# Kernel tuning notes

Hardware: AMD Instinct MI355X
Metric: run time of the kernel (lower is better)

## Reference

```python
import jax, jax.numpy as jnp
import numpy as np

N, E, F_IN, F_HID, F_EMB, N_CLS = 50000, 800000, 100, 100, 64, 40


def setup_inputs() -> dict:
    key = jax.random.key(0)
    ks = jax.random.split(key, 8)
    x = jax.random.normal(ks[0], (N, F_IN), dtype=jnp.float32)
    edge_index = jax.random.randint(ks[1], (2, E), 0, N, dtype=jnp.int32)
    W1 = jax.random.normal(ks[2], (F_IN, F_HID), dtype=jnp.float32) / np.sqrt(F_IN)
    b1 = jnp.zeros((F_HID,), dtype=jnp.float32)
    W2 = jax.random.normal(ks[3], (F_HID, F_EMB), dtype=jnp.float32) / np.sqrt(F_HID)
    b2 = jnp.zeros((F_EMB,), dtype=jnp.float32)
    Wc = jax.random.normal(ks[4], (F_EMB, N_CLS), dtype=jnp.float32) / np.sqrt(F_EMB)
    bc = jnp.zeros((N_CLS,), dtype=jnp.float32)
    return {"x": x, "edge_index": edge_index, "W1": W1, "b1": b1,
            "W2": W2, "b2": b2, "Wc": Wc, "bc": bc}


def _gcn_conv(x, W, b, src, dst, dinv):
    # linear transform then symmetric-normalized neighbor aggregation
    h = x @ W                                   # [N, out]
    norm = dinv[src] * dinv[dst]                # [E+N]
    msg = h[src] * norm[:, None]                # gather + scale (edge-wise)
    out = jax.ops.segment_sum(msg, dst, num_segments=x.shape[0])
    return out + b


def reference(x, edge_index, W1, b1, W2, b2, Wc, bc):
    x = x.astype(jnp.float32)
    n = x.shape[0]
    loop = jnp.arange(n, dtype=edge_index.dtype)
    src = jnp.concatenate([edge_index[0], loop])  # add self-loops (PyG GCNConv)
    dst = jnp.concatenate([edge_index[1], loop])
    # degree (with self-loops) and D^-1/2, shared by both conv layers
    deg = jax.ops.segment_sum(jnp.ones_like(dst, dtype=x.dtype), dst, num_segments=n)
    dinv = jnp.where(deg > 0, jax.lax.rsqrt(jnp.maximum(deg, 1e-12)), 0.0)
    h = jax.nn.relu(_gcn_conv(x, W1, b1, src, dst, dinv))   # dropout off (eval)
    h = _gcn_conv(h, W2, b2, src, dst, dinv)
    h = jax.nn.relu(h)                                      # dropout off (eval)
    return h @ Wc + bc
```

## Files before the change

### kernel.cpp

```cpp
#include <hip/hip_runtime.h>

#define FIN 100
#define FHID 100
#define FEMB 64
#define NCLS 40

#define BSH 6
#define NSEG 8
#define SEGCAP 224
#define CSTR 16

typedef __attribute__((ext_vector_type(8))) short short8;
typedef __attribute__((ext_vector_type(4))) float f32x4;

__device__ inline unsigned short f2bf(float f) {
    unsigned u = __float_as_uint(f);
    u += 0x7FFFu + ((u >> 16) & 1u);
    return (unsigned short)(u >> 16);
}
__device__ inline float bf2f(unsigned short s) {
    return __uint_as_float((unsigned)s << 16);
}
__device__ inline float4 bf4(ushort4 u) {
    return make_float4(bf2f(u.x), bf2f(u.y), bf2f(u.z), bf2f(u.w));
}

__global__ __launch_bounds__(256) void k_bucket_sort(const int* __restrict__ arena,
                                                     const int* __restrict__ cur,
                                                     int* __restrict__ gcounter,
                                                     int* __restrict__ rowptr,
                                                     int* __restrict__ rowend,
                                                     float* __restrict__ dinv,
                                                     int* __restrict__ src_sorted, int n) {
    const int b = blockIdx.x;
    __shared__ int cnt[64], off[64];
    __shared__ int base_sh;
    if (threadIdx.x < 64) cnt[threadIdx.x] = 0;
    __syncthreads();
    for (int s = 0; s < NSEG; ++s) {
        int len = cur[(b * NSEG + s) * CSTR];
        if (len > SEGCAP) len = SEGCAP;
        const int* seg = arena + (size_t)(b * NSEG + s) * SEGCAP;
        for (int idx = threadIdx.x; idx < len; idx += 256)
            atomicAdd(&cnt[seg[idx] & 63], 1);
    }
    __syncthreads();
    if (threadIdx.x == 0) {
        int run = 0;
        for (int j = 0; j < 64; ++j) { off[j] = run; run += cnt[j]; }
        base_sh = atomicAdd(gcounter, run);
    }
    __syncthreads();
    const int base = base_sh;
    if (threadIdx.x < 64) {
        int node = (b << BSH) + threadIdx.x;
        if (node < n) {
            int r0 = base + off[threadIdx.x];
            rowptr[node] = r0;
            rowend[node] = r0 + cnt[threadIdx.x];
            dinv[node] = rsqrtf((float)cnt[threadIdx.x] + 1.0f);
        }
    }
    __syncthreads();
    for (int s = 0; s < NSEG; ++s) {
        int len = cur[(b * NSEG + s) * CSTR];
        if (len > SEGCAP) len = SEGCAP;
        const int* seg = arena + (size_t)(b * NSEG + s) * SEGCAP;
        for (int idx = threadIdx.x; idx < len; idx += 256) {
            int v = seg[idx];
            int lpos = atomicAdd(&off[v & 63], 1);
            src_sorted[base + lpos] = v >> BSH;
        }
    }
}

template <int KIN, int KOUT, int NTY, bool A_BF16, bool BIAS, bool OUT_BF16, bool SCATTER>
__global__ __launch_bounds__(256) void k_gemm_mfma(const void* __restrict__ A,
                                                   const float* __restrict__ W,
                                                   const float* __restrict__ bias,
                                                   void* __restrict__ C, int n,
                                                   const int* __restrict__ src,
                                                   const int* __restrict__ dst,
                                                   int* __restrict__ cur,
                                                   int* __restrict__ arena, int E) {
    constexpr int KP    = ((KIN + 31) / 32) * 32;
    constexpr int NTALL = (KOUT + 15) / 16;
    constexpr int NTC   = NTY * 16;
    constexpr int APAD  = KP + 8;
    constexpr int NKC   = KP / 32;
    constexpr int TQ    = (NTY + 1) / 2;
    constexpr int KQ4   = KIN / 4;

    __shared__ unsigned short Abf[128 * APAD];
    __shared__ unsigned short Wt[NTC * APAD];

    const int row0 = blockIdx.x * 128;
    const int tid = threadIdx.x;

    if constexpr (SCATTER) {
        const int stride = gridDim.x * 256;
        for (int e = blockIdx.x * 256 + tid; e < E; e += stride) {
            int d = dst[e];
            int b = d >> BSH;
            int slot = b * NSEG + ((e >> 8) & (NSEG - 1));
            int p = atomicAdd(&cur[slot * CSTR], 1);
            if (p < SEGCAP) arena[slot * SEGCAP + p] = (src[e] << BSH) | (d & 63);
        }
    }

    if constexpr (A_BF16) {
        const ushort4* A4 = (const ushort4*)A;
        for (int idx = tid; idx < 128 * KQ4; idx += 256) {
            int r = idx / KQ4;
            int kq = idx - r * KQ4;
            ushort4 v = make_ushort4(0, 0, 0, 0);
            if (row0 + r < n) v = A4[(size_t)(row0 + r) * KQ4 + kq];
            *(ushort4*)&Abf[r * APAD + kq * 4] = v;
        }
    } else {
        const float* Af = (const float*)A;
        for (int idx = tid; idx < 128 * KQ4; idx += 256) {
            int r = idx / KQ4;
            int kq = idx - r * KQ4;
            float4 v = make_float4(0.f, 0.f, 0.f, 0.f);
            if (row0 + r < n) v = ((const float4*)(Af + (size_t)(row0 + r) * KIN))[kq];
            ushort4 o;
            o.x = f2bf(v.x); o.y = f2bf(v.y); o.z = f2bf(v.z); o.w = f2bf(v.w);
            *(ushort4*)&Abf[r * APAD + kq * 4] = o;
        }
    }
    if (KP > KIN) {
        constexpr int PADW = (KP > KIN) ? (KP - KIN) : 1;
        for (int idx = tid; idx < 128 * PADW; idx += 256) {
            int r = idx / PADW;
            Abf[r * APAD + KIN + (idx - r * PADW)] = 0;
        }
    }

    const int lane = tid & 63;
    const int w    = tid >> 6;
    const int m0   = (w >> 1) * 64;
    const int t0   = (w & 1) * TQ;
    const int lm   = lane & 15;
    const int quad = lane >> 4;

    for (int tb = 0; tb < NTALL; tb += NTY) {
        const int ntloc = (NTALL - tb < NTY) ? (NTALL - tb) : NTY;

        for (int idx = tid; idx < KIN * NTC; idx += 256) {
            int k = idx / NTC;
            int c = idx - k * NTC;
            int gc = tb * 16 + c;
            float v = (gc < KOUT) ? W[(size_t)k * KOUT + gc] : 0.f;
            Wt[c * APAD + k] = f2bf(v);
        }
        if (KP > KIN) {
            constexpr int PADW = (KP > KIN) ? (KP - KIN) : 1;
            for (int idx = tid; idx < NTC * PADW; idx += 256) {
                int c = idx / PADW;
                Wt[c * APAD + KIN + (idx - c * PADW)] = 0;
            }
        }
        __syncthreads();

        const int tcnt = (ntloc - t0 < TQ) ? (ntloc - t0) : TQ;

        f32x4 acc[4][TQ];
        #pragma unroll
        for (int i = 0; i < 4; ++i)
            #pragma unroll
            for (int t = 0; t < TQ; ++t)
                acc[i][t] = (f32x4)(0.f);

        for (int kt = 0; kt < NKC; ++kt) {
            short8 a[4], b[TQ];
            #pragma unroll
            for (int i = 0; i < 4; ++i)
                a[i] = *(const short8*)&Abf[(m0 + i * 16 + lm) * APAD + kt * 32 + quad * 8];
            #pragma unroll
            for (int t = 0; t < TQ; ++t)
                if (t < tcnt)
                    b[t] = *(const short8*)&Wt[((t0 + t) * 16 + lm) * APAD + kt * 32 + quad * 8];
            #pragma unroll
            for (int i = 0; i < 4; ++i)
                #pragma unroll
                for (int t = 0; t < TQ; ++t)
                    if (t < tcnt)
                        acc[i][t] = __builtin_amdgcn_mfma_f32_16x16x32_bf16(a[i], b[t], acc[i][t], 0, 0, 0);
        }

        #pragma unroll
        for (int t = 0; t < TQ; ++t) {
            if (t >= tcnt) continue;
            int col = (tb + t0 + t) * 16 + lm;
            if (col >= KOUT) continue;
            float bv = BIAS ? bias[col] : 0.f;
            #pragma unroll
            for (int i = 0; i < 4; ++i) {
                #pragma unroll
                for (int rg = 0; rg < 4; ++rg) {
                    int row = row0 + m0 + i * 16 + quad * 4 + rg;
                    if (row < n) {
                        float v = acc[i][t][rg] + bv;
                        if (OUT_BF16)
                            ((unsigned short*)C)[(size_t)row * KOUT + col] = f2bf(v);
                        else
                            ((float*)C)[(size_t)row * KOUT + col] = v;
                    }
                }
            }
        }
        __syncthreads();
    }
}

template <int F>
__global__ __launch_bounds__(256) void k_agg_bf(const unsigned short* __restrict__ h,
                                                const int* __restrict__ rowptr,
                                                const int* __restrict__ rowend,
                                                const int* __restrict__ src_sorted,
                                                const float* __restrict__ dinv,
                                                const float* __restrict__ bias,
                                                unsigned short* __restrict__ out, int n) {
    const int G = F / 4;
    int gid = blockIdx.x * blockDim.x + threadIdx.x;
    if (gid >= n * G) return;
    int i = gid / G;
    int cq = gid % G;
    const ushort4* h4 = (const ushort4*)h;

    float4 acc = make_float4(0.f, 0.f, 0.f, 0.f);
    int e = rowptr[i];
    const int end = rowend[i];
    for (; e + 3 < end; e += 4) {
        int s0 = src_sorted[e];
        int s1 = src_sorted[e + 1];
        int s2 = src_sorted[e + 2];
        int s3 = src_sorted[e + 3];
        ushort4 u0 = h4[(size_t)s0 * G + cq];
        ushort4 u1 = h4[(size_t)s1 * G + cq];
        ushort4 u2 = h4[(size_t)s2 * G + cq];
        ushort4 u3 = h4[(size_t)s3 * G + cq];
        float n0 = dinv[s0], n1 = dinv[s1], n2 = dinv[s2], n3 = dinv[s3];
        float4 v0 = bf4(u0), v1 = bf4(u1), v2 = bf4(u2), v3 = bf4(u3);
        acc.x = fmaf(v0.x, n0, acc.x); acc.y = fmaf(v0.y, n0, acc.y);
        acc.z = fmaf(v0.z, n0, acc.z); acc.w = fmaf(v0.w, n0, acc.w);
        acc.x = fmaf(v1.x, n1, acc.x); acc.y = fmaf(v1.y, n1, acc.y);
        acc.z = fmaf(v1.z, n1, acc.z); acc.w = fmaf(v1.w, n1, acc.w);
        acc.x = fmaf(v2.x, n2, acc.x); acc.y = fmaf(v2.y, n2, acc.y);
        acc.z = fmaf(v2.z, n2, acc.z); acc.w = fmaf(v2.w, n2, acc.w);
        acc.x = fmaf(v3.x, n3, acc.x); acc.y = fmaf(v3.y, n3, acc.y);
        acc.z = fmaf(v3.z, n3, acc.z); acc.w = fmaf(v3.w, n3, acc.w);
    }
    for (; e < end; ++e) {
        int s0 = src_sorted[e];
        float n0 = dinv[s0];
        float4 v0 = bf4(h4[(size_t)s0 * G + cq]);
        acc.x = fmaf(v0.x, n0, acc.x); acc.y = fmaf(v0.y, n0, acc.y);
        acc.z = fmaf(v0.z, n0, acc.z); acc.w = fmaf(v0.w, n0, acc.w);
    }

    float d = dinv[i];
    float4 hv = bf4(h4[(size_t)i * G + cq]);
    float4 bv = *(const float4*)&bias[cq * 4];
    ushort4 st;
    st.x = f2bf(fmaxf(fmaf(d, fmaf(d, hv.x, acc.x), bv.x), 0.f));
    st.y = f2bf(fmaxf(fmaf(d, fmaf(d, hv.y, acc.y), bv.y), 0.f));
    st.z = f2bf(fmaxf(fmaf(d, fmaf(d, hv.z, acc.z), bv.z), 0.f));
    st.w = f2bf(fmaxf(fmaf(d, fmaf(d, hv.w, acc.w), bv.w), 0.f));
    ((ushort4*)out)[(size_t)i * G + cq] = st;
}

extern "C" void kernel_launch(void* const* d_in, const int* in_sizes, int n_in,
                              void* d_out, int out_size, void* d_ws, size_t ws_size,
                              hipStream_t stream) {
    const float* x  = (const float*)d_in[0];
    const int*   ei = (const int*)d_in[1];
    const float* W1 = (const float*)d_in[2];
    const float* b1 = (const float*)d_in[3];
    const float* W2 = (const float*)d_in[4];
    const float* b2 = (const float*)d_in[5];
    const float* Wc = (const float*)d_in[6];
    const float* bc = (const float*)d_in[7];
    float* out = (float*)d_out;

    const int N = in_sizes[0] / FIN;
    const int E = in_sizes[1] / 2;
    const int* src = ei;
    const int* dst = ei + E;
    const int NBK = (N + 63) >> BSH;

    auto align = [](size_t v) { return (v + 255) & ~(size_t)255; };
    char* ws = (char*)d_ws;
    const size_t cur_bytes = align((size_t)NBK * NSEG * CSTR * 4 + 256);
    int*   cur        = (int*)ws;   ws += cur_bytes;
    int*   gcounter   = cur + (size_t)NBK * NSEG * CSTR;
    int*   arena      = (int*)ws;   ws += align((size_t)NBK * NSEG * SEGCAP * 4);
    int*   rowptr     = (int*)ws;   ws += align((size_t)N * 4);
    int*   rowend     = (int*)ws;   ws += align((size_t)N * 4);
    int*   src_sorted = (int*)ws;   ws += align((size_t)E * 4);
    float* dinv       = (float*)ws; ws += align((size_t)N * 4);
    unsigned short* h1  = (unsigned short*)ws; ws += align((size_t)N * FHID * 2);
    unsigned short* a1r = (unsigned short*)ws; ws += align((size_t)N * FHID * 2);
    unsigned short* h2  = (unsigned short*)ws; ws += align((size_t)N * FEMB * 2);
    unsigned short* a2r = (unsigned short*)ws; ws += align((size_t)N * FEMB * 2);

    const int B = 256;
    const int nmb = (N + 127) / 128;

    hipMemsetAsync(cur, 0, cur_bytes, stream);

    k_gemm_mfma<FIN, FHID, 4, false, false, true, true><<<nmb, B, 0, stream>>>(
        x, W1, nullptr, h1, N, src, dst, cur, arena, E);

    k_bucket_sort<<<NBK, B, 0, stream>>>(arena, cur, gcounter, rowptr, rowend, dinv, src_sorted, N);

    k_agg_bf<FHID><<<((size_t)N * (FHID / 4) + B - 1) / B, B, 0, stream>>>(
        h1, rowptr, rowend, src_sorted, dinv, b1, a1r, N);

    k_gemm_mfma<FHID, FEMB, 4, true, false, true, false><<<nmb, B, 0, stream>>>(
        a1r, W2, nullptr, h2, N, nullptr, nullptr, nullptr, nullptr, 0);

    k_agg_bf<FEMB><<<((size_t)N * (FEMB / 4) + B - 1) / B, B, 0, stream>>>(
        h2, rowptr, rowend, src_sorted, dinv, b2, a2r, N);

    k_gemm_mfma<FEMB, NCLS, 4, true, true, false, false><<<nmb, B, 0, stream>>>(
        a2r, Wc, bc, out, N, nullptr, nullptr, nullptr, nullptr, 0);
}
```

Before: 225.4 us.

## Replace fused per-edge global-atomic scatter with LDS-binned super-bucket scatter kernel

Edge binning moves out of the first GEMM into a dedicated kernel. Each block bins 2048 edges into 256-node super-buckets using shared-memory counters, then reserves space in the global arena with one atomic per bucket and writes records back coalesced. The bucket sort now processes one 256-node super-bucket per block, using a parallel prefix scan instead of a serial loop. The aim is to cut global atomic contention and scattered writes, at the cost of an extra launch and the loss of overlap between scattering and the GEMM. Capacity limits of 4608 per super-bucket could drop edges if degrees are skewed.

```diff
diff --git a/kernel.cpp b/kernel.cpp
--- a/kernel.cpp
+++ b/kernel.cpp
@@ -5,10 +5,11 @@
 #define FEMB 64
 #define NCLS 40
 
-#define BSH 6
-#define NSEG 8
-#define SEGCAP 224
+#define SBSH 8
+#define CAPB 24
+#define SBCAP 4608
 #define CSTR 16
+#define EPB 2048
 
 typedef __attribute__((ext_vector_type(8))) short short8;
 typedef __attribute__((ext_vector_type(4))) float f32x4;
@@ -25,64 +26,110 @@
     return make_float4(bf2f(u.x), bf2f(u.y), bf2f(u.z), bf2f(u.w));
 }
 
+__global__ __launch_bounds__(256) void k_scatter_bin(const int* __restrict__ src,
+                                                     const int* __restrict__ dst,
+                                                     int* __restrict__ gcur,
+                                                     int* __restrict__ arena,
+                                                     int E, int nsb) {
+    __shared__ int bins[256 * CAPB];
+    __shared__ int bcnt[256];
+    __shared__ int pbase[256];
+    const int tid = threadIdx.x;
+    bcnt[tid] = 0;
+    __syncthreads();
+
+    const int e0 = blockIdx.x * EPB;
+    #pragma unroll
+    for (int k = 0; k < EPB / 256; ++k) {
+        int e = e0 + k * 256 + tid;
+        if (e < E) {
+            int d = dst[e];
+            int sb = d >> SBSH;
+            int rec = (src[e] << SBSH) | (d & 255);
+            int c = atomicAdd(&bcnt[sb], 1);
+            if (c < CAPB) {
+                bins[sb * CAPB + c] = rec;
+            } else {
+                int p = atomicAdd(&gcur[sb * CSTR], 1);
+                if (p < SBCAP) arena[(size_t)sb * SBCAP + p] = rec;
+            }
+        }
+    }
+    __syncthreads();
+
+    if (tid < nsb) {
+        int c = bcnt[tid];
+        if (c > CAPB) c = CAPB;
+        pbase[tid] = (c > 0) ? atomicAdd(&gcur[tid * CSTR], c) : 0;
+    }
+    __syncthreads();
+
+    const int wv = tid >> 6, lane = tid & 63;
+    for (int sb = wv; sb < nsb; sb += 4) {
+        int c = bcnt[sb];
+        if (c > CAPB) c = CAPB;
+        int p = pbase[sb];
+        if (lane < c && p + lane < SBCAP)
+            arena[(size_t)sb * SBCAP + p + lane] = bins[sb * CAPB + lane];
+    }
+}
+
 __global__ __launch_bounds__(256) void k_bucket_sort(const int* __restrict__ arena,
-                                                     const int* __restrict__ cur,
+                                                     const int* __restrict__ gcur,
                                                      int* __restrict__ gcounter,
                                                      int* __restrict__ rowptr,
                                                      int* __restrict__ rowend,
                                                      float* __restrict__ dinv,
                                                      int* __restrict__ src_sorted, int n) {
-    const int b = blockIdx.x;
-    __shared__ int cnt[64], off[64];
+    const int sb = blockIdx.x;
+    const int tid = threadIdx.x;
+    __shared__ int cnt[256], off[256], tmp[256];
     __shared__ int base_sh;
-    if (threadIdx.x < 64) cnt[threadIdx.x] = 0;
-    __syncthreads();
-    for (int s = 0; s < NSEG; ++s) {
-        int len = cur[(b * NSEG + s) * CSTR];
-        if (len > SEGCAP) len = SEGCAP;
-        const int* seg = arena + (size_t)(b * NSEG + s) * SEGCAP;
-        for (int idx = threadIdx.x; idx < len; idx += 256)
-            atomicAdd(&cnt[seg[idx] & 63], 1);
-    }
-    __syncthreads();
-    if (threadIdx.x == 0) {
-        int run = 0;
-        for (int j = 0; j < 64; ++j) { off[j] = run; run += cnt[j]; }
-        base_sh = atomicAdd(gcounter, run);
-    }
-    __syncthreads();
+    cnt[tid] = 0;
+    __syncthreads();
+
+    int len = gcur[sb * CSTR];
+    if (len > SBCAP) len = SBCAP;
+    const int* seg = arena + (size_t)sb * SBCAP;
+    for (int i = tid; i < len; i += 256)
+        atomicAdd(&cnt[seg[i] & 255], 1);
+    __syncthreads();
+
+    const int v = cnt[tid];
+    tmp[tid] = v;
+    __syncthreads();
+    for (int o = 1; o < 256; o <<= 1) {
+        int t = (tid >= o) ? tmp[tid - o] : 0;
+        __syncthreads();
+        tmp[tid] += t;
+        __syncthreads();
+    }
+    off[tid] = tmp[tid] - v;
+    if (tid == 255) base_sh = atomicAdd(gcounter, tmp[255]);
+    __syncthreads();
+
     const int base = base_sh;
-    if (threadIdx.x < 64) {
-        int node = (b << BSH) + threadIdx.x;
-        if (node < n) {
-            int r0 = base + off[threadIdx.x];
-            rowptr[node] = r0;
-            rowend[node] = r0 + cnt[threadIdx.x];
-            dinv[node] = rsqrtf((float)cnt[threadIdx.x] + 1.0f);
-        }
-    }
-    __syncthreads();
-    for (int s = 0; s < NSEG; ++s) {
-        int len = cur[(b * NSEG + s) * CSTR];
-        if (len > SEGCAP) len = SEGCAP;
-        const int* seg = arena + (size_t)(b * NSEG + s) * SEGCAP;
-        for (int idx = threadIdx.x; idx < len; idx += 256) {
-            int v = seg[idx];
-            int lpos = atomicAdd(&off[v & 63], 1);
-            src_sorted[base + lpos] = v >> BSH;
-        }
-    }
-}
-
-template <int KIN, int KOUT, int NTY, bool A_BF16, bool BIAS, bool OUT_BF16, bool SCATTER>
+    int node = (sb << SBSH) + tid;
+    if (node < n) {
+        int r0 = base + off[tid];
+        rowptr[node] = r0;
+        rowend[node] = r0 + v;
+        dinv[node] = rsqrtf((float)v + 1.0f);
+    }
+    __syncthreads();
+
+    for (int i = tid; i < len; i += 256) {
+        int rec = seg[i];
+        int lpos = atomicAdd(&off[rec & 255], 1);
+        src_sorted[base + lpos] = rec >> SBSH;
+    }
+}
+
+template <int KIN, int KOUT, int NTY, bool A_BF16, bool BIAS, bool OUT_BF16>
 __global__ __launch_bounds__(256) void k_gemm_mfma(const void* __restrict__ A,
                                                    const float* __restrict__ W,
                                                    const float* __restrict__ bias,
-                                                   void* __restrict__ C, int n,
-                                                   const int* __restrict__ src,
-                                                   const int* __restrict__ dst,
-                                                   int* __restrict__ cur,
-                                                   int* __restrict__ arena, int E) {
+                                                   void* __restrict__ C, int n) {
     constexpr int KP    = ((KIN + 31) / 32) * 32;
     constexpr int NTALL = (KOUT + 15) / 16;
     constexpr int NTC   = NTY * 16;
@@ -96,17 +143,6 @@
 
     const int row0 = blockIdx.x * 128;
     const int tid = threadIdx.x;
-
-    if constexpr (SCATTER) {
-        const int stride = gridDim.x * 256;
-        for (int e = blockIdx.x * 256 + tid; e < E; e += stride) {
-            int d = dst[e];
-            int b = d >> BSH;
-            int slot = b * NSEG + ((e >> 8) & (NSEG - 1));
-            int p = atomicAdd(&cur[slot * CSTR], 1);
-            if (p < SEGCAP) arena[slot * SEGCAP + p] = (src[e] << BSH) | (d & 63);
-        }
-    }
 
     if constexpr (A_BF16) {
         const ushort4* A4 = (const ushort4*)A;
@@ -288,14 +324,14 @@
     const int E = in_sizes[1] / 2;
     const int* src = ei;
     const int* dst = ei + E;
-    const int NBK = (N + 63) >> BSH;
+    const int NSB = (N + 255) >> SBSH;
 
     auto align = [](size_t v) { return (v + 255) & ~(size_t)255; };
     char* ws = (char*)d_ws;
-    const size_t cur_bytes = align((size_t)NBK * NSEG * CSTR * 4 + 256);
-    int*   cur        = (int*)ws;   ws += cur_bytes;
-    int*   gcounter   = cur + (size_t)NBK * NSEG * CSTR;
-    int*   arena      = (int*)ws;   ws += align((size_t)NBK * NSEG * SEGCAP * 4);
+    const size_t cur_bytes = align((size_t)256 * CSTR * 4 + 256);
+    int*   gcur       = (int*)ws;   ws += cur_bytes;
+    int*   gcounter   = gcur + 256 * CSTR;
+    int*   arena      = (int*)ws;   ws += align((size_t)NSB * SBCAP * 4);
     int*   rowptr     = (int*)ws;   ws += align((size_t)N * 4);
     int*   rowend     = (int*)ws;   ws += align((size_t)N * 4);
     int*   src_sorted = (int*)ws;   ws += align((size_t)E * 4);
@@ -308,22 +344,21 @@
     const int B = 256;
     const int nmb = (N + 127) / 128;
 
-    hipMemsetAsync(cur, 0, cur_bytes, stream);
-
-    k_gemm_mfma<FIN, FHID, 4, false, false, true, true><<<nmb, B, 0, stream>>>(
-        x, W1, nullptr, h1, N, src, dst, cur, arena, E);
-
-    k_bucket_sort<<<NBK, B, 0, stream>>>(arena, cur, gcounter, rowptr, rowend, dinv, src_sorted, N);
+    hipMemsetAsync(gcur, 0, cur_bytes, stream);
+
+    k_scatter_bin<<<(E + EPB - 1) / EPB, B, 0, stream>>>(src, dst, gcur, arena, E, NSB);
+
+    k_bucket_sort<<<NSB, B, 0, stream>>>(arena, gcur, gcounter, rowptr, rowend, dinv, src_sorted, N);
+
+    k_gemm_mfma<FIN, FHID, 4, false, false, true><<<nmb, B, 0, stream>>>(x, W1, nullptr, h1, N);
 
     k_agg_bf<FHID><<<((size_t)N * (FHID / 4) + B - 1) / B, B, 0, stream>>>(
         h1, rowptr, rowend, src_sorted, dinv, b1, a1r, N);
 
-    k_gemm_mfma<FHID, FEMB, 4, true, false, true, false><<<nmb, B, 0, stream>>>(
-        a1r, W2, nullptr, h2, N, nullptr, nullptr, nullptr, nullptr, 0);
+    k_gemm_mfma<FHID, FEMB, 4, true, false, true><<<nmb, B, 0, stream>>>(a1r, W2, nullptr, h2, N);
 
     k_agg_bf<FEMB><<<((size_t)N * (FEMB / 4) + B - 1) / B, B, 0, stream>>>(
         h2, rowptr, rowend, src_sorted, dinv, b2, a2r, N);
 
-    k_gemm_mfma<FEMB, NCLS, 4, true, true, false, false><<<nmb, B, 0, stream>>>(
-        a2r, Wc, bc, out, N, nullptr, nullptr, nullptr, nullptr, 0);
-}
+    k_gemm_mfma<FEMB, NCLS, 4, true, true, false><<<nmb, B, 0, stream>>>(a2r, Wc, bc, out, N);
+}
```

After: 210.6 us. 1.07x faster.
